# Optimization experiments

Hardware: AMD Instinct MI355X
Metric: run time of the kernel (lower is better)

The kernel has to match this reference:

```python
import jax, jax.numpy as jnp
import numpy as np

B, N, C, H, W = 64, 500, 256, 64, 64


def grid_sample_bilinear(im, pts):
    """torch.grid_sample bilinear, align_corners=True, padding_mode='zeros'.
    im: [B,C,H,W]; pts: [B,N,2] (x,y) in [-1,1] -> [B,C,N]."""
    b, c, h, w = im.shape
    x = (pts[..., 0] + 1.0) * 0.5 * (w - 1)  # [B,N]
    y = (pts[..., 1] + 1.0) * 0.5 * (h - 1)
    x0 = jnp.floor(x); y0 = jnp.floor(y)
    x1 = x0 + 1.0; y1 = y0 + 1.0
    wx1 = x - x0; wx0 = 1.0 - wx1
    wy1 = y - y0; wy0 = 1.0 - wy1
    flat = im.reshape(b, c, h * w)

    def gather(xi, yi):
        inb = (xi >= 0) & (xi <= w - 1) & (yi >= 0) & (yi <= h - 1)
        xc = jnp.clip(xi, 0, w - 1).astype(jnp.int32)
        yc = jnp.clip(yi, 0, h - 1).astype(jnp.int32)
        idx = (yc * w + xc)[:, None, :]  # [B,1,N]
        g = jnp.take_along_axis(flat, idx, axis=2)  # [B,C,N]
        return g * inb[:, None, :].astype(im.dtype)

    return (gather(x0, y0) * (wx0 * wy0)[:, None, :]
            + gather(x1, y0) * (wx1 * wy0)[:, None, :]
            + gather(x0, y1) * (wx0 * wy1)[:, None, :]
            + gather(x1, y1) * (wx1 * wy1)[:, None, :])


def setup_inputs() -> dict:
    key = jax.random.key(0)
    ks = jax.random.split(key, 12)
    p = jax.random.uniform(ks[0], (B, N, 2), jnp.float32, -1.0, 1.0)
    s_feat = jax.random.normal(ks[1], (B, C, H, W), jnp.float32)
    def conv_p(k, co, ci):
        k1, k2 = jax.random.split(k)
        s = 1.0 / np.sqrt(ci)
        return (jax.random.uniform(k1, (co, ci), jnp.float32, -s, s),
                jax.random.uniform(k2, (co,), jnp.float32, -s, s))
    w0, b0 = conv_p(ks[2], 128, 256)
    w1, b1 = conv_p(ks[3], 64, 128 + 256)
    w2, b2 = conv_p(ks[4], 5, 64 + 256)
    fc_w, fc_b = conv_p(ks[5], 236, 5 * N)
    return {"p": p, "s_feat": s_feat, "w0": w0, "b0": b0, "w1": w1, "b1": b1,
            "w2": w2, "b2": b2, "fc_w": fc_w, "fc_b": fc_b}


def reference(p, s_feat, w0, b0, w1, b1, w2, b2, fc_w, fc_b):
    feat = grid_sample_bilinear(s_feat, p)  # [B,256,N]
    y = jnp.einsum('oc,bcn->bon', w0, feat) + b0[None, :, None]
    y = jax.nn.leaky_relu(y, 0.01)
    y = jnp.einsum('oc,bcn->bon', w1, jnp.concatenate([y, feat], axis=1)) + b1[None, :, None]
    y = jax.nn.leaky_relu(y, 0.01)
    y = jnp.einsum('oc,bcn->bon', w2, jnp.concatenate([y, feat], axis=1)) + b2[None, :, None]
    y = jax.nn.relu(y)           # last_op
    y = y.reshape(y.shape[0], -1)  # [B, 5*N]
    return y @ fc_w.T + fc_b       # [B, 236]
```

## Files before the change

kernel.cpp:

```cpp
#include <hip/hip_runtime.h>
#include <hip/hip_bf16.h>

#define BB 64
#define NN 500
#define CC 256
#define HH 64
#define WW 64
#define HWSZ 4096
#define NPTS 32000
#define NPAD 512

typedef __attribute__((ext_vector_type(4))) short s4v;
typedef __attribute__((ext_vector_type(8))) short s8v;
typedef __attribute__((ext_vector_type(4))) float f4v;
typedef __attribute__((ext_vector_type(4))) int i4v;

__device__ __forceinline__ unsigned short bfround(float f) {
    unsigned u = __builtin_bit_cast(unsigned, f);
    return (unsigned short)((u + 0x7FFFu + ((u >> 16) & 1u)) >> 16);
}

#define GATHER_BLKS 1024
#define NCHB 16
#define W0F_N 32768
#define W1F_N 24576
#define W2F_N 5120
#define PACK_N (W0F_N + W1F_N + W2F_N)
#define FCT_N 590000
#define PACKALL_N (PACK_N + FCT_N)
#define PACK_BLKS ((PACKALL_N + 511) / 512)

__global__ __launch_bounds__(512) void k_gp(const float* __restrict__ sfeat,
                                            const float* __restrict__ pts,
                                            const float* __restrict__ w0,
                                            const float* __restrict__ w1,
                                            const float* __restrict__ w2,
                                            const float* __restrict__ fcw,
                                            unsigned int* __restrict__ featB,
                                            unsigned short* __restrict__ w0f,
                                            unsigned short* __restrict__ w1f,
                                            unsigned short* __restrict__ w2f,
                                            float* __restrict__ fcwT) {
    __shared__ float im[2][HWSZ];
    const int blk = blockIdx.x;
    const int tid = threadIdx.x;

    if (blk >= GATHER_BLKS) {
        int i = (blk - GATHER_BLKS) * 512 + tid;
        if (i < W0F_N) {
            int j = i & 7, ll = (i >> 3) & 63, s = (i >> 9) & 7, m = i >> 12;
            int row = m * 16 + (ll & 15), k = s * 32 + (ll >> 4) * 8 + j;
            w0f[i] = bfround(w0[row * 256 + k]);
        } else if (i < W0F_N + W1F_N) {
            int d = i - W0F_N;
            int j = d & 7, ll = (d >> 3) & 63, rest = d >> 9;
            int s = rest % 12, m = rest / 12;
            int row = m * 16 + (ll & 15), k = s * 32 + (ll >> 4) * 8 + j;
            w1f[d] = bfround(w1[row * 384 + k]);
        } else if (i < PACK_N) {
            int d = i - (W0F_N + W1F_N);
            int j = d & 7, ll = (d >> 3) & 63, s = d >> 9;
            int row = ll & 15, k = s * 32 + (ll >> 4) * 8 + j;
            float v = (row < 5) ? w2[row * 320 + k] : 0.f;
            w2f[d] = bfround(v);
        } else if (i < PACKALL_N) {
            int d = i - PACK_N;
            int k = d / 236, o = d - k * 236;
            fcwT[d] = fcw[o * 2500 + k];
        }
        return;
    }

    const int b     = blk >> 4;
    const int chunk = blk & 15;
    const int ch0   = chunk * NCHB;
    const int n     = tid;

    int4 id = make_int4(0, 0, 0, 0);
    float4 wt = make_float4(0.f, 0.f, 0.f, 0.f);
    if (n < NN) {
        float x = (pts[((size_t)b * NN + n) * 2 + 0] + 1.f) * 0.5f * (float)(WW - 1);
        float y = (pts[((size_t)b * NN + n) * 2 + 1] + 1.f) * 0.5f * (float)(HH - 1);
        float x0f = floorf(x), y0f = floorf(y);
        float x1f = x0f + 1.f, y1f = y0f + 1.f;
        float wx1 = x - x0f, wx0 = 1.f - wx1;
        float wy1 = y - y0f, wy0 = 1.f - wy1;
        float mx0 = (x0f >= 0.f && x0f <= (float)(WW - 1)) ? 1.f : 0.f;
        float mx1 = (x1f >= 0.f && x1f <= (float)(WW - 1)) ? 1.f : 0.f;
        float my0 = (y0f >= 0.f && y0f <= (float)(HH - 1)) ? 1.f : 0.f;
        float my1 = (y1f >= 0.f && y1f <= (float)(HH - 1)) ? 1.f : 0.f;
        int x0 = (int)fminf(fmaxf(x0f, 0.f), (float)(WW - 1));
        int x1 = (int)fminf(fmaxf(x1f, 0.f), (float)(WW - 1));
        int y0 = (int)fminf(fmaxf(y0f, 0.f), (float)(HH - 1));
        int y1 = (int)fminf(fmaxf(y1f, 0.f), (float)(HH - 1));
        id = make_int4(y0 * WW + x0, y0 * WW + x1, y1 * WW + x0, y1 * WW + x1);
        wt = make_float4(wx0 * wy0 * mx0 * my0, wx1 * wy0 * mx1 * my0,
                         wx0 * wy1 * mx0 * my1, wx1 * wy1 * mx1 * my1);
    }

    const float4* src = (const float4*)(sfeat + ((size_t)b * CC + ch0) * HWSZ);

#pragma unroll
    for (int it = 0; it < 2; it++) {
        int j = it * 512 + tid;
        __builtin_amdgcn_global_load_lds(
            (const __attribute__((address_space(1))) void*)(src + j),
            (__attribute__((address_space(3))) void*)((float4*)im[0] + j),
            16, 0, 0);
    }

    unsigned short hprev = 0;
    for (int t = 0; t < NCHB; t++) {
        if (t + 1 < NCHB) {
            const float4* s2 = src + (size_t)(t + 1) * (HWSZ / 4);
            float4* dst = (float4*)im[(t + 1) & 1];
#pragma unroll
            for (int it = 0; it < 2; it++) {
                int j = it * 512 + tid;
                __builtin_amdgcn_global_load_lds(
                    (const __attribute__((address_space(1))) void*)(s2 + j),
                    (__attribute__((address_space(3))) void*)(dst + j),
                    16, 0, 0);
            }
            asm volatile("s_waitcnt vmcnt(2)" ::: "memory");
        } else {
            asm volatile("s_waitcnt vmcnt(0)" ::: "memory");
        }
        asm volatile("s_barrier" ::: "memory");

        if (n < NN) {
            const float* L = im[t & 1];
            float r = wt.x * L[id.x] + wt.y * L[id.y] + wt.z * L[id.z] + wt.w * L[id.w];
            unsigned short h = bfround(r);
            if (t & 1) {
                unsigned int v = (unsigned int)hprev | ((unsigned int)h << 16);
                int kg = chunk * 2 + (t >> 3);
                int jp = (t & 7) >> 1;
                featB[(((size_t)b * 32 + kg) * 4 + jp) * 512 + n] = v;
            } else {
                hprev = h;
            }
        }
        if (t + 1 < NCHB)
            asm volatile("s_barrier" ::: "memory");
    }
}

#define K1_S 136
#define K2_S 72

__device__ __forceinline__ s8v mkfrag(const unsigned short* p) {
    return *(const s8v*)p;
}

__global__ __launch_bounds__(512, 4) void k_mlp(const unsigned int* __restrict__ featB,
                                                const unsigned short* __restrict__ w0f,
                                                const unsigned short* __restrict__ w1f,
                                                const unsigned short* __restrict__ w2f,
                                                const float* __restrict__ b0,
                                                const float* __restrict__ b1,
                                                const float* __restrict__ b2,
                                                float* __restrict__ y2f) {
    __shared__ unsigned short c1B[32 * K1_S];
    __shared__ unsigned short c2B[32 * K2_S];

    const int b   = blockIdx.y;
    const int n0  = blockIdx.x * 32;
    const int tid = threadIdx.x;
    const int w   = tid >> 6, l = tid & 63;
    const int nt  = w & 1, mh = w >> 1;
    const int lo16 = l & 15, hi = l >> 4;
    const int c = nt * 16 + lo16;

    s8v bhs[8];
    const unsigned int* fb = featB + (size_t)b * (32 * 4 * 512) + (n0 + c);
#pragma unroll
    for (int s = 0; s < 8; s++) {
        const int kg = s * 4 + hi;
        i4v hx;
#pragma unroll
        for (int t = 0; t < 4; t++)
            hx[t] = (int)fb[(size_t)(kg * 4 + t) * 512];
        bhs[s] = __builtin_bit_cast(s8v, hx);
    }

    f4v acc0 = {0.f, 0.f, 0.f, 0.f}, acc1 = {0.f, 0.f, 0.f, 0.f};
#pragma unroll
    for (int s = 0; s < 8; s++) {
        const s8v a0 = mkfrag(w0f + ((size_t)((mh * 2) * 8 + s) * 64 + l) * 8);
        const s8v a1 = mkfrag(w0f + ((size_t)((mh * 2 + 1) * 8 + s) * 64 + l) * 8);
        acc0 = __builtin_amdgcn_mfma_f32_16x16x32_bf16(a0, bhs[s], acc0, 0, 0, 0);
        acc1 = __builtin_amdgcn_mfma_f32_16x16x32_bf16(a1, bhs[s], acc1, 0, 0, 0);
    }
#pragma unroll
    for (int m = 0; m < 2; m++) {
#pragma unroll
        for (int r = 0; r < 4; r++) {
            int ch = (mh * 2 + m) * 16 + hi * 4 + r;
            float v = (m ? acc1[r] : acc0[r]) + b0[ch];
            v = v > 0.f ? v : 0.01f * v;
            c1B[c * K1_S + ch] = bfround(v);
        }
    }
    __syncthreads();

    f4v accA = {0.f, 0.f, 0.f, 0.f};
#pragma unroll
    for (int s = 0; s < 4; s++) {
        const s8v bh = *(const s8v*)&c1B[c * K1_S + s * 32 + hi * 8];
        const s8v a  = mkfrag(w1f + ((size_t)(mh * 12 + s) * 64 + l) * 8);
        accA = __builtin_amdgcn_mfma_f32_16x16x32_bf16(a, bh, accA, 0, 0, 0);
    }
#pragma unroll
    for (int s = 4; s < 12; s++) {
        const s8v a = mkfrag(w1f + ((size_t)(mh * 12 + s) * 64 + l) * 8);
        accA = __builtin_amdgcn_mfma_f32_16x16x32_bf16(a, bhs[s - 4], accA, 0, 0, 0);
    }
#pragma unroll
    for (int r = 0; r < 4; r++) {
        int ch = mh * 16 + hi * 4 + r;
        float v = accA[r] + b1[ch];
        v = v > 0.f ? v : 0.01f * v;
        c2B[c * K2_S + ch] = bfround(v);
    }
    __syncthreads();

    if (mh == 0) {
        f4v acc2 = {0.f, 0.f, 0.f, 0.f};
#pragma unroll
        for (int s = 0; s < 2; s++) {
            const s8v bh = *(const s8v*)&c2B[c * K2_S + s * 32 + hi * 8];
            const s8v a  = mkfrag(w2f + ((size_t)s * 64 + l) * 8);
            acc2 = __builtin_amdgcn_mfma_f32_16x16x32_bf16(a, bh, acc2, 0, 0, 0);
        }
#pragma unroll
        for (int s = 2; s < 10; s++) {
            const s8v a = mkfrag(w2f + ((size_t)s * 64 + l) * 8);
            acc2 = __builtin_amdgcn_mfma_f32_16x16x32_bf16(a, bhs[s - 2], acc2, 0, 0, 0);
        }
#pragma unroll
        for (int r = 0; r < 4; r++) {
            int ch = hi * 4 + r;
            if (ch < 5) {
                float v = acc2[r] + b2[ch];
                v = fmaxf(v, 0.f);
                int n = n0 + c;
                if (n < NN) y2f[(size_t)b * 2500 + ch * NN + n] = v;
            }
        }
    }
}

__global__ __launch_bounds__(256) void k_fc1(const float* __restrict__ y2f,
                                             const float* __restrict__ fcwT,
                                             float* __restrict__ part) {
    __shared__ float ys[313];
    const int b  = blockIdx.x & 63;
    const int kc = blockIdx.x >> 6;
    const int start = kc * 312 + (kc < 4 ? kc : 4);
    const int len   = (kc < 4) ? 313 : 312;
    const float* yb = y2f + (size_t)b * 2500 + start;
    for (int j = threadIdx.x; j < len; j += 256) ys[j] = yb[j];
    __syncthreads();
    const int o = threadIdx.x;
    if (o < 236) {
        float acc = 0.f;
        const float* wp = fcwT + (size_t)start * 236 + o;
#pragma unroll 8
        for (int k = 0; k < len; k++) acc = fmaf(wp[(size_t)k * 236], ys[k], acc);
        part[((size_t)kc * 64 + b) * 236 + o] = acc;
    }
}

__global__ __launch_bounds__(256) void k_fc2(const float* __restrict__ part,
                                             const float* __restrict__ fcb,
                                             float* __restrict__ out) {
    const int b = blockIdx.x;
    const int o = threadIdx.x;
    if (o < 236) {
        float acc = fcb[o];
#pragma unroll
        for (int kc = 0; kc < 8; kc++) acc += part[((size_t)kc * 64 + b) * 236 + o];
        out[b * 236 + o] = acc;
    }
}

extern "C" void kernel_launch(void* const* d_in, const int* in_sizes, int n_in,
                              void* d_out, int out_size, void* d_ws, size_t ws_size,
                              hipStream_t stream) {
    const float* p   = (const float*)d_in[0];
    const float* sf  = (const float*)d_in[1];
    const float* w0  = (const float*)d_in[2];
    const float* b0  = (const float*)d_in[3];
    const float* w1  = (const float*)d_in[4];
    const float* b1  = (const float*)d_in[5];
    const float* w2  = (const float*)d_in[6];
    const float* b2  = (const float*)d_in[7];
    const float* fcw = (const float*)d_in[8];
    const float* fcb = (const float*)d_in[9];
    float* out = (float*)d_out;

    char* ws = (char*)d_ws;
    unsigned int*   featB = (unsigned int*)(ws);
    float*          y2f   = (float*)(ws + 16777216);
    float*          fcwT  = (float*)(ws + 17417216);
    float*          part  = (float*)(ws + 19777216);
    unsigned short* w0f   = (unsigned short*)(ws + 20260544);
    unsigned short* w1f   = (unsigned short*)(ws + 20326080);
    unsigned short* w2f   = (unsigned short*)(ws + 20375232);

    k_gp<<<GATHER_BLKS + PACK_BLKS, 512, 0, stream>>>(sf, p, w0, w1, w2, fcw,
                                                      featB, w0f, w1f, w2f, fcwT);
    k_mlp<<<dim3(16, BB), 512, 0, stream>>>(featB, w0f, w1f, w2f,
                                            b0, b1, b2, y2f);
    k_fc1<<<512, 256, 0, stream>>>(y2f, fcwT, part);
    k_fc2<<<BB, 256, 0, stream>>>(part, fcb, out);
}
```

Before: 82.89 us.

## Triple-buffer channel prefetch and halve channels per gather block

The grid-sample gather kernel now splits each batch into 32 channel chunks of 8 channels instead of 16 chunks of 16, doubling the number of gather blocks. It also uses a three-deep LDS ring buffer, keeping two channel planes in flight ahead of the one being sampled. This is meant to hide more of the HBM streaming latency of the feature maps and spread the load over more CUs. In exchange, LDS use per block rises to 48KB, which may lower occupancy, and each block has a shorter pipeline, so startup costs a larger share.

```diff
diff --git a/kernel.cpp b/kernel.cpp
--- a/kernel.cpp
+++ b/kernel.cpp
@@ -20,8 +20,9 @@
     return (unsigned short)((u + 0x7FFFu + ((u >> 16) & 1u)) >> 16);
 }
 
-#define GATHER_BLKS 1024
-#define NCHB 16
+#define GATHER_BLKS 2048
+#define NCHB 8
+#define NBUF 3
 #define W0F_N 32768
 #define W1F_N 24576
 #define W2F_N 5120
@@ -41,7 +42,7 @@
                                             unsigned short* __restrict__ w1f,
                                             unsigned short* __restrict__ w2f,
                                             float* __restrict__ fcwT) {
-    __shared__ float im[2][HWSZ];
+    __shared__ float im[NBUF][HWSZ];
     const int blk = blockIdx.x;
     const int tid = threadIdx.x;
 
@@ -71,8 +72,8 @@
         return;
     }
 
-    const int b     = blk >> 4;
-    const int chunk = blk & 15;
+    const int b     = blk >> 5;
+    const int chunk = blk & 31;
     const int ch0   = chunk * NCHB;
     const int n     = tid;
 
@@ -100,28 +101,29 @@
 
     const float4* src = (const float4*)(sfeat + ((size_t)b * CC + ch0) * HWSZ);
 
-#pragma unroll
-    for (int it = 0; it < 2; it++) {
-        int j = it * 512 + tid;
-        __builtin_amdgcn_global_load_lds(
-            (const __attribute__((address_space(1))) void*)(src + j),
-            (__attribute__((address_space(3))) void*)((float4*)im[0] + j),
-            16, 0, 0);
-    }
+#define ISSUE_CH(T, BUF)                                                      \
+    {                                                                         \
+        const float4* s2 = src + (size_t)(T) * (HWSZ / 4);                    \
+        float4* dst = (float4*)im[BUF];                                       \
+        _Pragma("unroll")                                                     \
+        for (int it = 0; it < 2; it++) {                                      \
+            int j = it * 512 + tid;                                           \
+            __builtin_amdgcn_global_load_lds(                                 \
+                (const __attribute__((address_space(1))) void*)(s2 + j),      \
+                (__attribute__((address_space(3))) void*)(dst + j),           \
+                16, 0, 0);                                                    \
+        }                                                                     \
+    }
+
+    ISSUE_CH(0, 0);
+    ISSUE_CH(1, 1);
 
     unsigned short hprev = 0;
     for (int t = 0; t < NCHB; t++) {
-        if (t + 1 < NCHB) {
-            const float4* s2 = src + (size_t)(t + 1) * (HWSZ / 4);
-            float4* dst = (float4*)im[(t + 1) & 1];
-#pragma unroll
-            for (int it = 0; it < 2; it++) {
-                int j = it * 512 + tid;
-                __builtin_amdgcn_global_load_lds(
-                    (const __attribute__((address_space(1))) void*)(s2 + j),
-                    (__attribute__((address_space(3))) void*)(dst + j),
-                    16, 0, 0);
-            }
+        if (t + 2 < NCHB) {
+            ISSUE_CH(t + 2, (t + 2) % 3);
+            asm volatile("s_waitcnt vmcnt(4)" ::: "memory");
+        } else if (t + 1 < NCHB) {
             asm volatile("s_waitcnt vmcnt(2)" ::: "memory");
         } else {
             asm volatile("s_waitcnt vmcnt(0)" ::: "memory");
@@ -129,14 +131,12 @@
         asm volatile("s_barrier" ::: "memory");
 
         if (n < NN) {
-            const float* L = im[t & 1];
+            const float* L = im[t % 3];
             float r = wt.x * L[id.x] + wt.y * L[id.y] + wt.z * L[id.z] + wt.w * L[id.w];
             unsigned short h = bfround(r);
             if (t & 1) {
                 unsigned int v = (unsigned int)hprev | ((unsigned int)h << 16);
-                int kg = chunk * 2 + (t >> 3);
-                int jp = (t & 7) >> 1;
-                featB[(((size_t)b * 32 + kg) * 4 + jp) * 512 + n] = v;
+                featB[(((size_t)b * 32 + chunk) * 4 + (t >> 1)) * 512 + n] = v;
             } else {
                 hprev = h;
             }
@@ -144,6 +144,7 @@
         if (t + 1 < NCHB)
             asm volatile("s_barrier" ::: "memory");
     }
+#undef ISSUE_CH
 }
 
 #define K1_S 136
```

After: 82.18 us. About the same (-0.9%).
